# Kernel optimization log

Hardware: AMD Instinct MI355X
Metric: run time of the kernel (lower is better)

## Reference

```python
import jax, jax.numpy as jnp
import numpy as np

B, T, D, H = 4, 2048, 1024, 16
HD = D // H  # head_dim = 64
ROPE_BASE = 10000.0


def rotate_half(x):
    # Faithful to source: interleaved rotate. x[..., ::2], x[..., 1::2]
    x1 = x[..., ::2]
    x2 = x[..., 1::2]
    return jnp.stack((-x2, x1), axis=-1).reshape(x.shape)


def rope_tables(seq_len, dim, dtype=jnp.float32):
    inv = 1.0 / (ROPE_BASE ** (jnp.arange(0, dim, 2, dtype=jnp.float32) / dim))
    t = jnp.arange(seq_len, dtype=jnp.float32)
    freqs = jnp.einsum('i,j->ij', t, inv)          # [T, dim/2]
    emb = jnp.concatenate((freqs, freqs), axis=-1)  # [T, dim]
    return jnp.cos(emb).astype(dtype)[None, None], jnp.sin(emb).astype(dtype)[None, None]


def setup_inputs() -> dict:
    key = jax.random.key(0)
    ks = jax.random.split(key, 9)
    s = 0.02
    return {
        'x':  jax.random.normal(ks[0], (B, T, D), jnp.float32),
        'Wq': jax.random.normal(ks[1], (D, D), jnp.float32) * s,
        'bq': jnp.zeros((D,), jnp.float32),
        'Wk': jax.random.normal(ks[2], (D, D), jnp.float32) * s,
        'bk': jnp.zeros((D,), jnp.float32),
        'Wv': jax.random.normal(ks[3], (D, D), jnp.float32) * s,
        'bv': jnp.zeros((D,), jnp.float32),
        'Wo': jax.random.normal(ks[4], (D, D), jnp.float32) * s,
        'bo': jnp.zeros((D,), jnp.float32),
    }


def reference(x, Wq, bq, Wk, bk, Wv, bv, Wo, bo):
    b, t, d = x.shape
    # QKV projections -> [B, H, T, HD]
    def proj(W, bias):
        return (x @ W.T + bias).reshape(b, t, H, HD).transpose(0, 2, 1, 3)
    q, k, v = proj(Wq, bq), proj(Wk, bk), proj(Wv, bv)
    # RoPE (as written in source: non-interleaved cos/sin with interleaved rotate_half)
    cos, sin = rope_tables(t, HD, x.dtype)
    q = q * cos + rotate_half(q) * sin
    k = k * cos + rotate_half(k) * sin
    # Attention
    scale = 1.0 / jnp.sqrt(jnp.asarray(HD, x.dtype))
    attn = jnp.einsum('bhqd,bhkd->bhqk', q, k) * scale
    attn = jax.nn.softmax(attn, axis=-1)
    out = jnp.einsum('bhqk,bhkd->bhqd', attn, v)
    out = out.transpose(0, 2, 1, 3).reshape(b, t, d)
    return out @ Wo.T + bo
```

## Files before the change

### kernel.cpp

```cpp
#include <hip/hip_runtime.h>
#include <hip/hip_bf16.h>

constexpr int Bb = 4, Tt = 2048, Dd = 1024, Hh = 16, HD = 64;
constexpr int Mm = Bb * Tt;

typedef __attribute__((ext_vector_type(8))) short bf16x8;
typedef __attribute__((ext_vector_type(4))) short s16x4;
typedef __attribute__((ext_vector_type(4))) float f32x4;
typedef __attribute__((ext_vector_type(16))) float f32x16;

__device__ __forceinline__ short f2bf(float f) {
  union { float f; unsigned u; } v; v.f = f;
  unsigned r = (v.u + 0x7fffu + ((v.u >> 16) & 1u)) >> 16;
  return (short)r;
}

__device__ __forceinline__ unsigned cvt_pk_bf16(float lo, float hi) {
  unsigned r;
  asm("v_cvt_pk_bf16_f32 %0, %1, %2" : "=v"(r) : "v"(lo), "v"(hi));
  return r;
}

__device__ __forceinline__ float max3f(float a, float b, float c) {
  float d;
  asm("v_max3_f32 %0, %1, %2, %3" : "=v"(d) : "v"(a), "v"(b), "v"(c));
  return d;
}

__device__ __forceinline__ void gl_lds16(const short* gsrc, short* ldst) {
  __builtin_amdgcn_global_load_lds(
      (const __attribute__((address_space(1))) void*)gsrc,
      (__attribute__((address_space(3))) void*)ldst, 16, 0, 0);
}

__global__ __launch_bounds__(256) void cvt_k(const float* __restrict__ src,
                                             short* __restrict__ dst, int n4) {
  int i = blockIdx.x * 256 + threadIdx.x;
  if (i >= n4) return;
  float4 v = ((const float4*)src)[i];
  s16x4 p = { f2bf(v.x), f2bf(v.y), f2bf(v.z), f2bf(v.w) };
  ((s16x4*)dst)[i] = p;
}

__global__ void rope_tab(float* __restrict__ cs, float* __restrict__ sn) {
  int idx = blockIdx.x * 256 + threadIdx.x;
  if (idx >= Tt * HD) return;
  int t = idx >> 6, d = idx & (HD - 1);
  float f = powf(10000.0f, -(float)(d & 31) / 32.0f);
  float ang = (float)t * f;
  cs[idx] = cosf(ang);
  sn[idx] = sinf(ang);
}

__global__ __launch_bounds__(256) void gemm_qk(
    const short* __restrict__ Ab,
    const short* __restrict__ Wqb, const short* __restrict__ Wkb,
    const float* __restrict__ bq, const float* __restrict__ bk,
    short* __restrict__ Qo, short* __restrict__ Ko,
    const float* __restrict__ cs, const float* __restrict__ sn)
{
  constexpr int K = 1024;
  __shared__ short Alds[128 * 64];
  __shared__ short Blds[128 * 64];
  const bool isQ = (blockIdx.z == 0);
  const short* Wb = isQ ? Wqb : Wkb;
  const float* bias = isQ ? bq : bk;
  short* outb = isQ ? Qo : Ko;
  const float scale = isQ ? 0.18033688f : 1.0f;

  const int tid = threadIdx.x;
  const int lane = tid & 63, wave = tid >> 6;
  const int g = lane >> 4, li = lane & 15;
  const int m0 = blockIdx.x * 128, n0 = blockIdx.y * 128;
  const int wm = (wave >> 1) * 64, wn = (wave & 1) * 64;
  f32x4 acc[4][4] = {};

  const int lrow = lane >> 3;
  const int soff = lrow * K + (((lane & 7) ^ lrow) * 8);
  const short* Asrc = Ab + (size_t)(m0 + wave * 32) * K + soff;
  const short* Bsrc = Wb + (size_t)(n0 + wave * 32) * K + soff;
  short* Adst = Alds + wave * 32 * 64;
  short* Bdst = Blds + wave * 32 * 64;

  for (int k0 = 0; k0 < K; k0 += 64) {
    #pragma unroll
    for (int i = 0; i < 4; i++) {
      gl_lds16(Asrc + (size_t)i * 8 * K + k0, Adst + i * 8 * 64);
      gl_lds16(Bsrc + (size_t)i * 8 * K + k0, Bdst + i * 8 * 64);
    }
    __syncthreads();

    bf16x8 af[4][2], bfr[4][2];
    #pragma unroll
    for (int i = 0; i < 4; i++) {
      int row = wm + i * 16 + li, sw = li & 7;
      #pragma unroll
      for (int kk = 0; kk < 2; kk++)
        af[i][kk] = *(const bf16x8*)&Alds[row * 64 + (((kk * 4 + g) ^ sw) * 8)];
    }
    #pragma unroll
    for (int j = 0; j < 4; j++) {
      int row = wn + j * 16 + li, sw = li & 7;
      #pragma unroll
      for (int kk = 0; kk < 2; kk++)
        bfr[j][kk] = *(const bf16x8*)&Blds[row * 64 + (((kk * 4 + g) ^ sw) * 8)];
    }
    #pragma unroll
    for (int i = 0; i < 4; i++)
      #pragma unroll
      for (int j = 0; j < 4; j++)
        #pragma unroll
        for (int kk = 0; kk < 2; kk++)
          acc[i][j] = __builtin_amdgcn_mfma_f32_16x16x32_bf16(
              af[i][kk], bfr[j][kk], acc[i][j], 0, 0, 0);
    __syncthreads();
  }

  #pragma unroll
  for (int i = 0; i < 4; i++)
    #pragma unroll
    for (int j = 0; j < 4; j++)
      #pragma unroll
      for (int r = 0; r < 4; r++) {
        int m = m0 + wm + i * 16 + g * 4 + r;
        int n = n0 + wn + j * 16 + li;
        float val = acc[i][j][r] + bias[n];
        float partner = __shfl_xor(val, 1, 64);
        int tt = m & (Tt - 1), hd = n & (HD - 1);
        float c = cs[tt * HD + hd], s = sn[tt * HD + hd];
        float rh = (n & 1) ? partner : -partner;
        val = (val * c + rh * s) * scale;
        int bI = m >> 11, h = n >> 6;
        outb[(((size_t)bI * Hh + h) * Tt + tt) * HD + hd] = f2bf(val);
      }
}

__global__ __launch_bounds__(256) void gemm_fin(
    const short* __restrict__ Ab, const short* __restrict__ Wb,
    const float* __restrict__ bias, float* __restrict__ outf)
{
  constexpr int K = 1024;
  __shared__ short Alds[128 * 64];
  __shared__ short Blds[128 * 64];
  const int tid = threadIdx.x;
  const int lane = tid & 63, wave = tid >> 6;
  const int g = lane >> 4, li = lane & 15;
  const int m0 = blockIdx.x * 128, n0 = blockIdx.y * 128;
  const int wm = (wave >> 1) * 64, wn = (wave & 1) * 64;
  f32x4 acc[4][4] = {};

  const int lrow = lane >> 3;
  const int soff = lrow * K + (((lane & 7) ^ lrow) * 8);
  const short* Asrc = Ab + (size_t)(m0 + wave * 32) * K + soff;
  const short* Bsrc = Wb + (size_t)(n0 + wave * 32) * K + soff;
  short* Adst = Alds + wave * 32 * 64;
  short* Bdst = Blds + wave * 32 * 64;

  for (int k0 = 0; k0 < K; k0 += 64) {
    #pragma unroll
    for (int i = 0; i < 4; i++) {
      gl_lds16(Asrc + (size_t)i * 8 * K + k0, Adst + i * 8 * 64);
      gl_lds16(Bsrc + (size_t)i * 8 * K + k0, Bdst + i * 8 * 64);
    }
    __syncthreads();

    bf16x8 af[4][2], bfr[4][2];
    #pragma unroll
    for (int i = 0; i < 4; i++) {
      int row = wm + i * 16 + li, sw = li & 7;
      #pragma unroll
      for (int kk = 0; kk < 2; kk++)
        af[i][kk] = *(const bf16x8*)&Alds[row * 64 + (((kk * 4 + g) ^ sw) * 8)];
    }
    #pragma unroll
    for (int j = 0; j < 4; j++) {
      int row = wn + j * 16 + li, sw = li & 7;
      #pragma unroll
      for (int kk = 0; kk < 2; kk++)
        bfr[j][kk] = *(const bf16x8*)&Blds[row * 64 + (((kk * 4 + g) ^ sw) * 8)];
    }
    #pragma unroll
    for (int i = 0; i < 4; i++)
      #pragma unroll
      for (int j = 0; j < 4; j++)
        #pragma unroll
        for (int kk = 0; kk < 2; kk++)
          acc[i][j] = __builtin_amdgcn_mfma_f32_16x16x32_bf16(
              af[i][kk], bfr[j][kk], acc[i][j], 0, 0, 0);
    __syncthreads();
  }

  #pragma unroll
  for (int i = 0; i < 4; i++)
    #pragma unroll
    for (int j = 0; j < 4; j++)
      #pragma unroll
      for (int r = 0; r < 4; r++) {
        int m = m0 + wm + i * 16 + g * 4 + r;
        int n = n0 + wn + j * 16 + li;
        outf[(size_t)m * Dd + n] = acc[i][j][r] + bias[n];
      }
}

__global__ __launch_bounds__(256) void gemm_v(
    const short* __restrict__ Ab, const float* __restrict__ Wf,
    const float* __restrict__ bias, short* __restrict__ outb)
{
  constexpr int K = 1024;
  __shared__ short Alds[128][72];
  __shared__ short Blds[128][72];
  const int tid = threadIdx.x;
  const int lane = tid & 63, wave = tid >> 6;
  const int g = lane >> 4, li = lane & 15;
  const int m0 = blockIdx.x * 128, n0 = blockIdx.y * 128;
  const int wm = (wave >> 1) * 64, wn = (wave & 1) * 64;
  f32x4 acc[4][4] = {};

  for (int k0 = 0; k0 < K; k0 += 64) {
    #pragma unroll
    for (int s = 0; s < 4; s++) {
      int f = tid + s * 256; int row = f >> 3, c8 = f & 7;
      *(bf16x8*)&Alds[row][c8 * 8] =
          *(const bf16x8*)(Ab + (size_t)(m0 + row) * K + k0 + c8 * 8);
    }
    #pragma unroll
    for (int s = 0; s < 8; s++) {
      int f = tid + s * 256; int row = f >> 4, c4 = f & 15;
      float4 v = *(const float4*)(Wf + (size_t)(n0 + row) * K + k0 + c4 * 4);
      s16x4 p = { f2bf(v.x), f2bf(v.y), f2bf(v.z), f2bf(v.w) };
      *(s16x4*)&Blds[row][c4 * 4] = p;
    }
    __syncthreads();

    bf16x8 af[4][2], bfr[4][2];
    #pragma unroll
    for (int i = 0; i < 4; i++)
      #pragma unroll
      for (int kk = 0; kk < 2; kk++)
        af[i][kk] = *(const bf16x8*)&Alds[wm + i * 16 + li][kk * 32 + g * 8];
    #pragma unroll
    for (int j = 0; j < 4; j++)
      #pragma unroll
      for (int kk = 0; kk < 2; kk++)
        bfr[j][kk] = *(const bf16x8*)&Blds[wn + j * 16 + li][kk * 32 + g * 8];
    #pragma unroll
    for (int i = 0; i < 4; i++)
      #pragma unroll
      for (int j = 0; j < 4; j++)
        #pragma unroll
        for (int kk = 0; kk < 2; kk++)
          acc[i][j] = __builtin_amdgcn_mfma_f32_16x16x32_bf16(
              af[i][kk], bfr[j][kk], acc[i][j], 0, 0, 0);
    __syncthreads();
  }

  #pragma unroll
  for (int i = 0; i < 4; i++)
    #pragma unroll
    for (int j = 0; j < 4; j++) {
      int n = n0 + wn + j * 16 + li;
      s16x4 pk;
      #pragma unroll
      for (int r = 0; r < 4; r++) pk[r] = f2bf(acc[i][j][r] + bias[n]);
      int mb = m0 + wm + i * 16 + g * 4;
      int bI = mb >> 11, t0 = mb & (Tt - 1), h = n >> 6, d = n & (HD - 1);
      *(s16x4*)(outb + (((size_t)bI * Hh + h) * HD + d) * Tt + t0) = pk;
    }
}

__device__ __forceinline__ void store_o(const f32x16& o, float inv,
                                        short* __restrict__ AO, size_t rowbase,
                                        int colbase, int h) {
  #pragma unroll
  for (int R = 0; R < 4; R++) {
    s16x4 pk;
    #pragma unroll
    for (int j = 0; j < 4; j++) pk[j] = f2bf(o[R * 4 + j] * inv);
    *(s16x4*)(AO + rowbase + colbase + 8 * R + 4 * h) = pk;
  }
}

__global__ __launch_bounds__(128, 4) void attn_k(
    const short* __restrict__ Qb, const short* __restrict__ Kb,
    const short* __restrict__ Vt_g, short* __restrict__ AO)
{
  __shared__ short Klds[64][72];
  __shared__ short Vt[64][72];
  const int tid = threadIdx.x, lane = tid & 63, wave = tid >> 6;
  const int h = lane >> 5;
  const int ql = lane & 31;
  const int bh = blockIdx.x;
  const int q0 = blockIdx.y * 64 + wave * 32;
  const size_t base  = (size_t)bh * Tt * HD;
  const size_t basev = (size_t)bh * HD * Tt;

  bf16x8 qf[4];
  #pragma unroll
  for (int ks = 0; ks < 4; ks++)
    qf[ks] = *(const bf16x8*)(Qb + base + (size_t)(q0 + ql) * HD + ks * 16 + h * 8);

  float m_i = -3.0e38f, l_i = 0.f;
  f32x16 o0 = {}, o1 = {};

  for (int kv0 = 0; kv0 < Tt; kv0 += 64) {
    #pragma unroll
    for (int s = 0; s < 4; s++) {
      int f = tid + s * 128; int row = f >> 3, c8 = f & 7;
      *(bf16x8*)&Klds[row][c8 * 8] =
          *(const bf16x8*)(Kb + base + (size_t)(kv0 + row) * HD + c8 * 8);
      *(bf16x8*)&Vt[row][c8 * 8] =
          *(const bf16x8*)(Vt_g + basev + (size_t)row * Tt + kv0 + c8 * 8);
    }
    __syncthreads();

    f32x16 st0 = {}, st1 = {};
    __builtin_amdgcn_s_setprio(1);
    #pragma unroll
    for (int ks = 0; ks < 4; ks++) {
      bf16x8 kf0 = *(const bf16x8*)&Klds[ql][ks * 16 + h * 8];
      bf16x8 kf1 = *(const bf16x8*)&Klds[32 + ql][ks * 16 + h * 8];
      st0 = __builtin_amdgcn_mfma_f32_32x32x16_bf16(kf0, qf[ks], st0, 0, 0, 0);
      st1 = __builtin_amdgcn_mfma_f32_32x32x16_bf16(kf1, qf[ks], st1, 0, 0, 0);
    }
    __builtin_amdgcn_s_setprio(0);

    float t0 = max3f(st0[0],  st0[1],  st0[2]);
    float t1 = max3f(st0[3],  st0[4],  st0[5]);
    float t2 = max3f(st0[6],  st0[7],  st0[8]);
    float t3 = max3f(st0[9],  st0[10], st0[11]);
    float t4 = max3f(st0[12], st0[13], st0[14]);
    float t5 = max3f(st0[15], st1[0],  st1[1]);
    float t6 = max3f(st1[2],  st1[3],  st1[4]);
    float t7 = max3f(st1[5],  st1[6],  st1[7]);
    float t8 = max3f(st1[8],  st1[9],  st1[10]);
    float t9 = max3f(st1[11], st1[12], st1[13]);
    float ta = fmaxf(st1[14], st1[15]);
    float u0 = max3f(t0, t1, t2);
    float u1 = max3f(t3, t4, t5);
    float u2 = max3f(t6, t7, t8);
    float u3 = fmaxf(t9, ta);
    float mv = fmaxf(max3f(u0, u1, u2), u3);
    mv = fmaxf(mv, __shfl_xor(mv, 32, 64));

    if (!__all(mv <= m_i + 8.0f)) {
      float mn = fmaxf(m_i, mv);
      float corr = __builtin_amdgcn_exp2f(m_i - mn);
      m_i = mn;
      l_i *= corr;
      #pragma unroll
      for (int r = 0; r < 16; r++) { o0[r] *= corr; o1[r] *= corr; }
    }

    float rs = 0.f;
    #pragma unroll
    for (int r = 0; r < 16; r++) { st0[r] = __builtin_amdgcn_exp2f(st0[r] - m_i); rs += st0[r]; }
    #pragma unroll
    for (int r = 0; r < 16; r++) { st1[r] = __builtin_amdgcn_exp2f(st1[r] - m_i); rs += st1[r]; }
    rs += __shfl_xor(rs, 32, 64);
    l_i += rs;

    __builtin_amdgcn_s_setprio(1);
    #pragma unroll
    for (int ks = 0; ks < 4; ks++) {
      const int b0 = ((2 * ks) & 3) * 4;
      float A0, A1, A2, A3, B0, B1, B2, B3;
      if (ks < 2) {
        A0 = st0[b0]; A1 = st0[b0 + 1]; A2 = st0[b0 + 2]; A3 = st0[b0 + 3];
        B0 = st0[b0 + 4]; B1 = st0[b0 + 5]; B2 = st0[b0 + 6]; B3 = st0[b0 + 7];
      } else {
        A0 = st1[b0]; A1 = st1[b0 + 1]; A2 = st1[b0 + 2]; A3 = st1[b0 + 3];
        B0 = st1[b0 + 4]; B1 = st1[b0 + 5]; B2 = st1[b0 + 6]; B3 = st1[b0 + 7];
      }
      unsigned wa0 = cvt_pk_bf16(A0, A1), wa1 = cvt_pk_bf16(A2, A3);
      unsigned wb0 = cvt_pk_bf16(B0, B1), wb1 = cvt_pk_bf16(B2, B3);
      unsigned s0 = h ? wa0 : wb0, s1 = h ? wa1 : wb1;
      unsigned r0 = (unsigned)__shfl_xor((int)s0, 32, 64);
      unsigned r1 = (unsigned)__shfl_xor((int)s1, 32, 64);
      unsigned own0 = h ? wb0 : wa0, own1 = h ? wb1 : wa1;
      union { unsigned u[4]; bf16x8 v; } pa;
      pa.u[0] = h ? r0 : own0;  pa.u[1] = h ? r1 : own1;
      pa.u[2] = h ? own0 : r0;  pa.u[3] = h ? own1 : r1;

      bf16x8 vf0 = *(const bf16x8*)&Vt[ql][ks * 16 + h * 8];
      bf16x8 vf1 = *(const bf16x8*)&Vt[32 + ql][ks * 16 + h * 8];
      o0 = __builtin_amdgcn_mfma_f32_32x32x16_bf16(vf0, pa.v, o0, 0, 0, 0);
      o1 = __builtin_amdgcn_mfma_f32_32x32x16_bf16(vf1, pa.v, o1, 0, 0, 0);
    }
    __builtin_amdgcn_s_setprio(0);
    __syncthreads();
  }

  float inv = 1.0f / l_i;
  const int b = bh >> 4, hh = bh & 15;
  size_t rowbase = ((size_t)b * Tt + q0 + ql) * Dd;
  store_o(o0, inv, AO, rowbase, hh * 64 + 0, h);
  store_o(o1, inv, AO, rowbase, hh * 64 + 32, h);
}

extern "C" void kernel_launch(void* const* d_in, const int* in_sizes, int n_in,
                              void* d_out, int out_size, void* d_ws, size_t ws_size,
                              hipStream_t stream)
{
  const float* x  = (const float*)d_in[0];
  const float* Wq = (const float*)d_in[1];
  const float* bq = (const float*)d_in[2];
  const float* Wk = (const float*)d_in[3];
  const float* bk = (const float*)d_in[4];
  const float* Wv = (const float*)d_in[5];
  const float* bv = (const float*)d_in[6];
  const float* Wo = (const float*)d_in[7];
  const float* bo = (const float*)d_in[8];
  float* out = (float*)d_out;

  char* ws = (char*)d_ws;
  float* cs = (float*)ws;
  float* sn = (float*)(ws + (size_t)(1 << 19));
  char*  p0 = ws + ((size_t)1 << 20);
  short* Qb = (short*)(p0);
  short* Kb = (short*)(p0 + ((size_t)16 << 20));
  short* Vb = (short*)(p0 + ((size_t)32 << 20));
  short* xb = (short*)(p0 + ((size_t)48 << 20));
  short* AO  = xb;
  short* Wqb = Vb;
  short* Wkb = (short*)(p0 + ((size_t)34 << 20));
  short* Wob = Kb;

  cvt_k<<<dim3(Mm * Dd / 4 / 256), dim3(256), 0, stream>>>(x,  xb,  Mm * Dd / 4);
  cvt_k<<<dim3(Dd * Dd / 4 / 256), dim3(256), 0, stream>>>(Wq, Wqb, Dd * Dd / 4);
  cvt_k<<<dim3(Dd * Dd / 4 / 256), dim3(256), 0, stream>>>(Wk, Wkb, Dd * Dd / 4);
  rope_tab<<<dim3(512), dim3(256), 0, stream>>>(cs, sn);

  dim3 bb(256);
  gemm_qk<<<dim3(Mm / 128, Dd / 128, 2), bb, 0, stream>>>(
      xb, Wqb, Wkb, bq, bk, Qb, Kb, cs, sn);
  gemm_v<<<dim3(Mm / 128, Dd / 128), bb, 0, stream>>>(xb, Wv, bv, Vb);

  attn_k<<<dim3(Bb * Hh, Tt / 64), dim3(128), 0, stream>>>(Qb, Kb, Vb, AO);

  cvt_k<<<dim3(Dd * Dd / 4 / 256), dim3(256), 0, stream>>>(Wo, Wob, Dd * Dd / 4);
  gemm_fin<<<dim3(Mm / 128, Dd / 128), bb, 0, stream>>>(AO, Wob, bo, out);
}
```

Before: 224.4 us.

## Fuse V projection into QK GEMM and prefetch K/V tiles in attention

Merges the separate V projection GEMM into the Q/K GEMM launch as a third z-slice. The merged kernel uses pre-converted bf16 weights staged in the output buffer, converted by a single three-way conversion kernel. The attention kernel now loads the next K/V tile into registers while computing the current one, then writes it to LDS between barriers. This removes a launch and the slower fp32-weight V GEMM, and hides global load latency in attention, at the cost of extra registers and an additional barrier per iteration.

New measurement: 269.9 us. 1.2x slower.

```diff
diff --git a/kernel.cpp b/kernel.cpp
--- a/kernel.cpp
+++ b/kernel.cpp
@@ -37,6 +37,18 @@
                                              short* __restrict__ dst, int n4) {
   int i = blockIdx.x * 256 + threadIdx.x;
   if (i >= n4) return;
+  float4 v = ((const float4*)src)[i];
+  s16x4 p = { f2bf(v.x), f2bf(v.y), f2bf(v.z), f2bf(v.w) };
+  ((s16x4*)dst)[i] = p;
+}
+
+__global__ __launch_bounds__(256) void cvt3_k(
+    const float* __restrict__ s0, const float* __restrict__ s1,
+    const float* __restrict__ s2,
+    short* __restrict__ d0, short* __restrict__ d1, short* __restrict__ d2) {
+  const float* src = blockIdx.y == 0 ? s0 : blockIdx.y == 1 ? s1 : s2;
+  short* dst = blockIdx.y == 0 ? d0 : blockIdx.y == 1 ? d1 : d2;
+  int i = blockIdx.x * 256 + threadIdx.x;
   float4 v = ((const float4*)src)[i];
   s16x4 p = { f2bf(v.x), f2bf(v.y), f2bf(v.z), f2bf(v.w) };
   ((s16x4*)dst)[i] = p;
@@ -52,21 +64,22 @@
   sn[idx] = sinf(ang);
 }
 
-__global__ __launch_bounds__(256) void gemm_qk(
+__global__ __launch_bounds__(256) void gemm_qkv(
     const short* __restrict__ Ab,
     const short* __restrict__ Wqb, const short* __restrict__ Wkb,
+    const short* __restrict__ Wvb,
     const float* __restrict__ bq, const float* __restrict__ bk,
-    short* __restrict__ Qo, short* __restrict__ Ko,
+    const float* __restrict__ bv,
+    short* __restrict__ Qo, short* __restrict__ Ko, short* __restrict__ Vo,
     const float* __restrict__ cs, const float* __restrict__ sn)
 {
   constexpr int K = 1024;
   __shared__ short Alds[128 * 64];
   __shared__ short Blds[128 * 64];
-  const bool isQ = (blockIdx.z == 0);
-  const short* Wb = isQ ? Wqb : Wkb;
-  const float* bias = isQ ? bq : bk;
-  short* outb = isQ ? Qo : Ko;
-  const float scale = isQ ? 0.18033688f : 1.0f;
+  const int z = blockIdx.z;
+  const short* Wb = z == 0 ? Wqb : z == 1 ? Wkb : Wvb;
+  const float* bias = z == 0 ? bq : z == 1 ? bk : bv;
+  short* outb = z == 0 ? Qo : z == 1 ? Ko : Vo;
 
   const int tid = threadIdx.x;
   const int lane = tid & 63, wave = tid >> 6;
@@ -116,23 +129,39 @@
     __syncthreads();
   }
 
-  #pragma unroll
-  for (int i = 0; i < 4; i++)
-    #pragma unroll
-    for (int j = 0; j < 4; j++)
-      #pragma unroll
-      for (int r = 0; r < 4; r++) {
-        int m = m0 + wm + i * 16 + g * 4 + r;
+  if (z == 2) {
+    #pragma unroll
+    for (int i = 0; i < 4; i++)
+      #pragma unroll
+      for (int j = 0; j < 4; j++) {
         int n = n0 + wn + j * 16 + li;
-        float val = acc[i][j][r] + bias[n];
-        float partner = __shfl_xor(val, 1, 64);
-        int tt = m & (Tt - 1), hd = n & (HD - 1);
-        float c = cs[tt * HD + hd], s = sn[tt * HD + hd];
-        float rh = (n & 1) ? partner : -partner;
-        val = (val * c + rh * s) * scale;
-        int bI = m >> 11, h = n >> 6;
-        outb[(((size_t)bI * Hh + h) * Tt + tt) * HD + hd] = f2bf(val);
+        s16x4 pk;
+        #pragma unroll
+        for (int r = 0; r < 4; r++) pk[r] = f2bf(acc[i][j][r] + bias[n]);
+        int mb = m0 + wm + i * 16 + g * 4;
+        int bI = mb >> 11, t0 = mb & (Tt - 1), h = n >> 6, d = n & (HD - 1);
+        *(s16x4*)(outb + (((size_t)bI * Hh + h) * HD + d) * Tt + t0) = pk;
       }
+  } else {
+    const float scale = z == 0 ? 0.18033688f : 1.0f;
+    #pragma unroll
+    for (int i = 0; i < 4; i++)
+      #pragma unroll
+      for (int j = 0; j < 4; j++)
+        #pragma unroll
+        for (int r = 0; r < 4; r++) {
+          int m = m0 + wm + i * 16 + g * 4 + r;
+          int n = n0 + wn + j * 16 + li;
+          float val = acc[i][j][r] + bias[n];
+          float partner = __shfl_xor(val, 1, 64);
+          int tt = m & (Tt - 1), hd = n & (HD - 1);
+          float c = cs[tt * HD + hd], s = sn[tt * HD + hd];
+          float rh = (n & 1) ? partner : -partner;
+          val = (val * c + rh * s) * scale;
+          int bI = m >> 11, h = n >> 6;
+          outb[(((size_t)bI * Hh + h) * Tt + tt) * HD + hd] = f2bf(val);
+        }
+  }
 }
 
 __global__ __launch_bounds__(256) void gemm_fin(
@@ -202,72 +231,6 @@
       }
 }
 
-__global__ __launch_bounds__(256) void gemm_v(
-    const short* __restrict__ Ab, const float* __restrict__ Wf,
-    const float* __restrict__ bias, short* __restrict__ outb)
-{
-  constexpr int K = 1024;
-  __shared__ short Alds[128][72];
-  __shared__ short Blds[128][72];
-  const int tid = threadIdx.x;
-  const int lane = tid & 63, wave = tid >> 6;
-  const int g = lane >> 4, li = lane & 15;
-  const int m0 = blockIdx.x * 128, n0 = blockIdx.y * 128;
-  const int wm = (wave >> 1) * 64, wn = (wave & 1) * 64;
-  f32x4 acc[4][4] = {};
-
-  for (int k0 = 0; k0 < K; k0 += 64) {
-    #pragma unroll
-    for (int s = 0; s < 4; s++) {
-      int f = tid + s * 256; int row = f >> 3, c8 = f & 7;
-      *(bf16x8*)&Alds[row][c8 * 8] =
-          *(const bf16x8*)(Ab + (size_t)(m0 + row) * K + k0 + c8 * 8);
-    }
-    #pragma unroll
-    for (int s = 0; s < 8; s++) {
-      int f = tid + s * 256; int row = f >> 4, c4 = f & 15;
-      float4 v = *(const float4*)(Wf + (size_t)(n0 + row) * K + k0 + c4 * 4);
-      s16x4 p = { f2bf(v.x), f2bf(v.y), f2bf(v.z), f2bf(v.w) };
-      *(s16x4*)&Blds[row][c4 * 4] = p;
-    }
-    __syncthreads();
-
-    bf16x8 af[4][2], bfr[4][2];
-    #pragma unroll
-    for (int i = 0; i < 4; i++)
-      #pragma unroll
-      for (int kk = 0; kk < 2; kk++)
-        af[i][kk] = *(const bf16x8*)&Alds[wm + i * 16 + li][kk * 32 + g * 8];
-    #pragma unroll
-    for (int j = 0; j < 4; j++)
-      #pragma unroll
-      for (int kk = 0; kk < 2; kk++)
-        bfr[j][kk] = *(const bf16x8*)&Blds[wn + j * 16 + li][kk * 32 + g * 8];
-    #pragma unroll
-    for (int i = 0; i < 4; i++)
-      #pragma unroll
-      for (int j = 0; j < 4; j++)
-        #pragma unroll
-        for (int kk = 0; kk < 2; kk++)
-          acc[i][j] = __builtin_amdgcn_mfma_f32_16x16x32_bf16(
-              af[i][kk], bfr[j][kk], acc[i][j], 0, 0, 0);
-    __syncthreads();
-  }
-
-  #pragma unroll
-  for (int i = 0; i < 4; i++)
-    #pragma unroll
-    for (int j = 0; j < 4; j++) {
-      int n = n0 + wn + j * 16 + li;
-      s16x4 pk;
-      #pragma unroll
-      for (int r = 0; r < 4; r++) pk[r] = f2bf(acc[i][j][r] + bias[n]);
-      int mb = m0 + wm + i * 16 + g * 4;
-      int bI = mb >> 11, t0 = mb & (Tt - 1), h = n >> 6, d = n & (HD - 1);
-      *(s16x4*)(outb + (((size_t)bI * Hh + h) * HD + d) * Tt + t0) = pk;
-    }
-}
-
 __device__ __forceinline__ void store_o(const f32x16& o, float inv,
                                         short* __restrict__ AO, size_t rowbase,
                                         int colbase, int h) {
@@ -302,16 +265,31 @@
   float m_i = -3.0e38f, l_i = 0.f;
   f32x16 o0 = {}, o1 = {};
 
-  for (int kv0 = 0; kv0 < Tt; kv0 += 64) {
-    #pragma unroll
-    for (int s = 0; s < 4; s++) {
-      int f = tid + s * 128; int row = f >> 3, c8 = f & 7;
-      *(bf16x8*)&Klds[row][c8 * 8] =
-          *(const bf16x8*)(Kb + base + (size_t)(kv0 + row) * HD + c8 * 8);
-      *(bf16x8*)&Vt[row][c8 * 8] =
-          *(const bf16x8*)(Vt_g + basev + (size_t)row * Tt + kv0 + c8 * 8);
-    }
-    __syncthreads();
+  const int srow = tid >> 3, sc8 = (tid & 7) * 8;
+  bf16x8 kreg[4], vreg[4];
+
+  #pragma unroll
+  for (int s = 0; s < 4; s++) {
+    kreg[s] = *(const bf16x8*)(Kb + base + (size_t)(srow + s * 16) * HD + sc8);
+    vreg[s] = *(const bf16x8*)(Vt_g + basev + (size_t)(srow + s * 16) * Tt + sc8);
+  }
+  #pragma unroll
+  for (int s = 0; s < 4; s++) {
+    *(bf16x8*)&Klds[srow + s * 16][sc8] = kreg[s];
+    *(bf16x8*)&Vt[srow + s * 16][sc8] = vreg[s];
+  }
+  __syncthreads();
+
+  constexpr int NT = Tt / 64;
+  for (int t = 0; t < NT; t++) {
+    if (t + 1 < NT) {
+      int kv1 = (t + 1) * 64;
+      #pragma unroll
+      for (int s = 0; s < 4; s++) {
+        kreg[s] = *(const bf16x8*)(Kb + base + (size_t)(kv1 + srow + s * 16) * HD + sc8);
+        vreg[s] = *(const bf16x8*)(Vt_g + basev + (size_t)(srow + s * 16) * Tt + kv1 + sc8);
+      }
+    }
 
     f32x16 st0 = {}, st1 = {};
     __builtin_amdgcn_s_setprio(1);
@@ -387,7 +365,16 @@
       o1 = __builtin_amdgcn_mfma_f32_32x32x16_bf16(vf1, pa.v, o1, 0, 0, 0);
     }
     __builtin_amdgcn_s_setprio(0);
-    __syncthreads();
+
+    if (t + 1 < NT) {
+      __syncthreads();
+      #pragma unroll
+      for (int s = 0; s < 4; s++) {
+        *(bf16x8*)&Klds[srow + s * 16][sc8] = kreg[s];
+        *(bf16x8*)&Vt[srow + s * 16][sc8] = vreg[s];
+      }
+      __syncthreads();
+    }
   }
 
   float inv = 1.0f / l_i;
@@ -421,22 +408,21 @@
   short* Vb = (short*)(p0 + ((size_t)32 << 20));
   short* xb = (short*)(p0 + ((size_t)48 << 20));
   short* AO  = xb;
-  short* Wqb = Vb;
-  short* Wkb = (short*)(p0 + ((size_t)34 << 20));
   short* Wob = Kb;
-
-  cvt_k<<<dim3(Mm * Dd / 4 / 256), dim3(256), 0, stream>>>(x,  xb,  Mm * Dd / 4);
-  cvt_k<<<dim3(Dd * Dd / 4 / 256), dim3(256), 0, stream>>>(Wq, Wqb, Dd * Dd / 4);
-  cvt_k<<<dim3(Dd * Dd / 4 / 256), dim3(256), 0, stream>>>(Wk, Wkb, Dd * Dd / 4);
+  short* Wqb = (short*)d_out;
+  short* Wkb = (short*)d_out + ((size_t)1 << 20);
+  short* Wvb = (short*)d_out + ((size_t)2 << 20);
+
+  cvt_k<<<dim3(Mm * Dd / 4 / 256), dim3(256), 0, stream>>>(x, xb, Mm * Dd / 4);
+  cvt3_k<<<dim3(Dd * Dd / 4 / 256, 3), dim3(256), 0, stream>>>(
+      Wq, Wk, Wv, Wqb, Wkb, Wvb);
   rope_tab<<<dim3(512), dim3(256), 0, stream>>>(cs, sn);
 
-  dim3 bb(256);
-  gemm_qk<<<dim3(Mm / 128, Dd / 128, 2), bb, 0, stream>>>(
-      xb, Wqb, Wkb, bq, bk, Qb, Kb, cs, sn);
-  gemm_v<<<dim3(Mm / 128, Dd / 128), bb, 0, stream>>>(xb, Wv, bv, Vb);
+  gemm_qkv<<<dim3(Mm / 128, Dd / 128, 3), dim3(256), 0, stream>>>(
+      xb, Wqb, Wkb, Wvb, bq, bk, bv, Qb, Kb, Vb, cs, sn);
 
   attn_k<<<dim3(Bb * Hh, Tt / 64), dim3(128), 0, stream>>>(Qb, Kb, Vb, AO);
 
   cvt_k<<<dim3(Dd * Dd / 4 / 256), dim3(256), 0, stream>>>(Wo, Wob, Dd * Dd / 4);
-  gemm_fin<<<dim3(Mm / 128, Dd / 128), bb, 0, stream>>>(AO, Wob, bo, out);
-}
+  gemm_fin<<<dim3(Mm / 128, Dd / 128), dim3(256), 0, stream>>>(AO, Wob, bo, out);
+}
```
